# Optimization experiments

Hardware: AMD Instinct MI355X
Metric: run time of the kernel (lower is better)

Reference implementation:

```python
import jax, jax.numpy as jnp
import numpy as np
from jax import lax

B, LAT, NCLS, NGF, NC = 256, 100, 10, 128, 3
EPS = 1e-5


def _convt(x, w, stride, pad):
    # torch ConvTranspose2d(weight shape (Cin,Cout,k,k)) == lhs-dilated conv
    # with spatially flipped, in/out-swapped kernel and padding k-1-pad.
    k = w.shape[2]
    wt = jnp.flip(w, (2, 3)).transpose(1, 0, 2, 3)  # (Cout, Cin, k, k)
    p = k - 1 - pad
    return lax.conv_general_dilated(x, wt, (1, 1), [(p, p), (p, p)],
                                    lhs_dilation=(stride, stride),
                                    dimension_numbers=('NCHW', 'OIHW', 'NCHW'))


def _cconvt(xr, xi, wr, wi, br, bi, stride, pad):
    # complex transposed conv decomposed into 4 real convs (as torch does)
    yr = _convt(xr, wr, stride, pad) - _convt(xi, wi, stride, pad) + br[None, :, None, None]
    yi = _convt(xr, wi, stride, pad) + _convt(xi, wr, stride, pad) + bi[None, :, None, None]
    return yr, yi


def _cbn(xr, xi, grr, gri, gii, br, bi):
    # complex batchnorm: 2x2 covariance whitening over (N,H,W) + affine
    ax = (0, 2, 3)
    bc = lambda v: v[None, :, None, None]
    xr = xr - bc(xr.mean(ax))
    xi = xi - bc(xi.mean(ax))
    crr = (xr * xr).mean(ax) + EPS
    cii = (xi * xi).mean(ax) + EPS
    cri = (xr * xi).mean(ax)
    s = jnp.sqrt(crr * cii - cri * cri)          # sqrt(det)
    t = jnp.sqrt(crr + cii + 2.0 * s)            # sqrt(trace + 2 sqrt(det))
    inv = 1.0 / (s * t)
    rrr = (cii + s) * inv
    rii = (crr + s) * inv
    rri = -cri * inv
    yr = bc(rrr) * xr + bc(rri) * xi
    yi = bc(rri) * xr + bc(rii) * xi
    out_r = bc(grr) * yr + bc(gri) * yi + bc(br)
    out_i = bc(gri) * yr + bc(gii) * yi + bc(bi)
    return out_r, out_i


def _forward(noise_re, noise_im, labels, emb,
             w1r, w1i, b1r, b1i, g1rr, g1ri, g1ii, n1br, n1bi,
             w2r, w2i, b2r, b2i, g2rr, g2ri, g2ii, n2br, n2bi,
             w3r, w3i, b3r, b3i, g3rr, g3ri, g3ii, n3br, n3bi,
             w4r, w4i, b4r, b4i):
    lab = emb[labels][:, :, None, None]  # (B, NCLS, 1, 1); embedding is real
    xr = jnp.concatenate([noise_re, lab], axis=1)
    xi = jnp.concatenate([noise_im, jnp.zeros_like(lab)], axis=1)
    # 1x1 -> 4x4
    xr, xi = _cconvt(xr, xi, w1r, w1i, b1r, b1i, 1, 0)
    xr, xi = _cbn(xr, xi, g1rr, g1ri, g1ii, n1br, n1bi)
    xr, xi = jax.nn.relu(xr), jax.nn.relu(xi)  # CReLU
    # 4x4 -> 8x8
    xr, xi = _cconvt(xr, xi, w2r, w2i, b2r, b2i, 2, 1)
    xr, xi = _cbn(xr, xi, g2rr, g2ri, g2ii, n2br, n2bi)
    xr, xi = jax.nn.relu(xr), jax.nn.relu(xi)
    # 8x8 -> 16x16
    xr, xi = _cconvt(xr, xi, w3r, w3i, b3r, b3i, 2, 1)
    xr, xi = _cbn(xr, xi, g3rr, g3ri, g3ii, n3br, n3bi)
    xr, xi = jax.nn.relu(xr), jax.nn.relu(xi)
    # 16x16 -> 32x32
    xr, xi = _cconvt(xr, xi, w4r, w4i, b4r, b4i, 2, 1)
    return jnp.tanh(xr), jnp.tanh(xi)  # CTanh


def setup_inputs() -> dict:
    key = jax.random.key(0)
    ks = iter(jax.random.split(key, 40))
    rn = lambda shape, s: jax.random.normal(next(ks), shape, jnp.float32) * s
    d = {}
    d['noise_re'] = rn((B, LAT, 1, 1), 1.0)
    d['noise_im'] = rn((B, LAT, 1, 1), 1.0)
    d['labels'] = jax.random.randint(next(ks), (B,), 0, NCLS, jnp.int32)
    d['emb'] = rn((NCLS, NCLS), 1.0)
    chans = [(LAT + NCLS, NGF * 4), (NGF * 4, NGF * 2), (NGF * 2, NGF), (NGF, NC)]
    for i, (ci, co) in enumerate(chans, 1):
        d[f'w{i}r'] = rn((ci, co, 4, 4), 0.02)
        d[f'w{i}i'] = rn((ci, co, 4, 4), 0.02)
        d[f'b{i}r'] = jnp.zeros((co,), jnp.float32)
        d[f'b{i}i'] = jnp.zeros((co,), jnp.float32)
        if i < 4:
            d[f'g{i}rr'] = jnp.full((co,), 0.70710678, jnp.float32)
            d[f'g{i}ri'] = jnp.zeros((co,), jnp.float32)
            d[f'g{i}ii'] = jnp.full((co,), 0.70710678, jnp.float32)
            d[f'n{i}br'] = jnp.zeros((co,), jnp.float32)
            d[f'n{i}bi'] = jnp.zeros((co,), jnp.float32)
    return d


def reference(noise_re, noise_im, labels, emb,
              w1r, w1i, b1r, b1i, g1rr, g1ri, g1ii, n1br, n1bi,
              w2r, w2i, b2r, b2i, g2rr, g2ri, g2ii, n2br, n2bi,
              w3r, w3i, b3r, b3i, g3rr, g3ri, g3ii, n3br, n3bi,
              w4r, w4i, b4r, b4i):
    out_r, out_i = _forward(noise_re, noise_im, labels, emb,
                            w1r, w1i, b1r, b1i, g1rr, g1ri, g1ii, n1br, n1bi,
                            w2r, w2i, b2r, b2i, g2rr, g2ri, g2ii, n2br, n2bi,
                            w3r, w3i, b3r, b3i, g3rr, g3ri, g3ii, n3br, n3bi,
                            w4r, w4i, b4r, b4i)
    return out_r + 1j * out_i  # complex64 (B, NC, 32, 32)
```

## Files before the change

### kernel.cpp

```cpp
#include <hip/hip_runtime.h>
#include <hip/hip_bf16.h>
#include <math.h>

#define BATCH 256
#define LAT 100
#define NCLS 10
#define CIN0 110
#define C1 512
#define C2 256
#define C3 128
#define NCH 3
#define EPS 1e-5f

typedef __hip_bfloat16 bf16;
typedef short bf16x8 __attribute__((ext_vector_type(8)));
typedef float f32x4 __attribute__((ext_vector_type(4)));

__device__ __forceinline__ float b2f(bf16 v) { return __bfloat162float(v); }
__device__ __forceinline__ bf16 f2b(float v) { return __float2bfloat16(v); }
__device__ __forceinline__ float s2f(short s) {
    unsigned u = ((unsigned)(unsigned short)s) << 16;
    return __builtin_bit_cast(float, u);
}
__device__ __forceinline__ short f2s(float f) {
    bf16 b = __float2bfloat16(f);
    return *(short*)&b;
}

#define NB_W1 14336
#define NB_W2 32768
#define NB_W3 8192
#define NB_W4 256
#define NB_X0 224

__device__ __forceinline__ void w1prep_body(const float* wr, const float* wi, bf16* B, int idx) {
    if (idx >= 16384 * 224) return;
    int n = idx / 224, k = idx - n * 224;
    int p = n >> 10, cop = n & 1023;
    int pk = k >= 112; int ci = k - pk * 112;
    float v = 0.f;
    if (ci < CIN0) {
        int co = (cop < C1) ? cop : cop - C1;
        size_t widx = ((size_t)ci * C1 + co) * 16 + p;
        float vr = wr[widx], vi = wi[widx];
        v = (cop < C1) ? (pk ? -vi : vr) : (pk ? vr : vi);
    }
    B[idx] = f2b(v);
}

template<int CIN, int N>
__device__ __forceinline__ void wprep_panel_body(const float* wr, const float* wi, bf16* W,
                                                 size_t idx) {
    constexpr int K = 4 * CIN, TWOK = 8 * CIN;
    size_t per_cls = (size_t)2 * N * TWOK;
    if (idx >= 4 * per_cls) return;
    int cls = (int)(idx / per_cls);
    size_t r = idx - (size_t)cls * per_cls;
    size_t chunk_nb = (size_t)TWOK * 128;
    int nb = (int)(r / chunk_nb);
    int r2 = (int)(r - (size_t)nb * chunk_nb);
    int kb = r2 >> 12;
    int w = r2 & 4095;
    int f = w >> 9;
    int l = (w >> 3) & 63;
    int j = w & 7;
    int n = nb * 128 + (f >> 2) * 64 + (f & 3) * 16 + (l & 15);
    int k = kb * 32 + (l >> 4) * 8 + j;
    int py = cls >> 1, px = cls & 1;
    int p = k >= K; int kk = k - p * K;
    int t = kk / CIN, ci = kk - t * CIN;
    int a = t >> 1, e = t & 1;
    int kh = py ? (a ? 2 : 0) : (a ? 3 : 1);
    int kw = px ? (e ? 2 : 0) : (e ? 3 : 1);
    int co = (n < N) ? n : n - N;
    size_t widx = ((size_t)ci * N + co) * 16 + kh * 4 + kw;
    float vr = wr[widx], vi = wi[widx];
    float v = (n < N) ? (p ? -vi : vr) : (p ? vr : vi);
    W[idx] = f2b(v);
}

__device__ __forceinline__ void wprep4_body(const float* wr, const float* wi, bf16* W, int idx) {
    if (idx >= 65536) return;
    int cls = idx >> 14, rem = idx & 16383;
    int py = cls >> 1, px = cls & 1;
    int n = rem >> 10, k = rem & 1023;
    float v = 0.f;
    if (n < NCH) {
        int p = k >= 512; int kk = k - p * 512;
        int t = kk >> 7, ci = kk & 127;
        int a = t >> 1, e = t & 1;
        int kh = py ? (a ? 2 : 0) : (a ? 3 : 1);
        int kw = px ? (e ? 2 : 0) : (e ? 3 : 1);
        size_t widx = ((size_t)ci * NCH + n) * 16 + kh * 4 + kw;
        v = p ? -wi[widx] : wr[widx];
    }
    W[idx] = f2b(v);
}

__device__ __forceinline__ void x0_body(const float* nre, const float* nim,
                                        const int* labels, const float* emb,
                                        bf16* A, int idx) {
    if (idx >= BATCH * 224) return;
    int b = idx / 224, k = idx - b * 224;
    int p = k >= 112; int ci = k - p * 112;
    float v = 0.f;
    if (ci < CIN0) {
        if (!p) v = (ci < LAT) ? nre[b * LAT + ci] : emb[labels[b] * NCLS + (ci - LAT)];
        else    v = (ci < LAT) ? nim[b * LAT + ci] : 0.f;
    }
    A[idx] = f2b(v);
}

__global__ void prep_combined(const float* __restrict__ w1r, const float* __restrict__ w1i,
                              const float* __restrict__ w2r, const float* __restrict__ w2i,
                              const float* __restrict__ w3r, const float* __restrict__ w3i,
                              const float* __restrict__ w4r, const float* __restrict__ w4i,
                              const float* __restrict__ nre, const float* __restrict__ nim,
                              const int* __restrict__ labels, const float* __restrict__ emb,
                              bf16* __restrict__ B1, bf16* __restrict__ W2all,
                              bf16* __restrict__ W3all, bf16* __restrict__ W4all,
                              bf16* __restrict__ x0bf) {
    int bid = blockIdx.x;
    if (bid < NB_W1) {
        w1prep_body(w1r, w1i, B1, bid * 256 + threadIdx.x);
    } else if (bid < NB_W1 + NB_W2) {
        wprep_panel_body<C1, C2>(w2r, w2i, W2all, (size_t)(bid - NB_W1) * 256 + threadIdx.x);
    } else if (bid < NB_W1 + NB_W2 + NB_W3) {
        wprep_panel_body<C2, C3>(w3r, w3i, W3all, (size_t)(bid - NB_W1 - NB_W2) * 256 + threadIdx.x);
    } else if (bid < NB_W1 + NB_W2 + NB_W3 + NB_W4) {
        wprep4_body(w4r, w4i, W4all, (bid - NB_W1 - NB_W2 - NB_W3) * 256 + threadIdx.x);
    } else {
        x0_body(nre, nim, labels, emb, x0bf,
                (bid - NB_W1 - NB_W2 - NB_W3 - NB_W4) * 256 + threadIdx.x);
    }
}

__global__ __launch_bounds__(256, 1) void gemm1(
    const bf16* __restrict__ A, const bf16* __restrict__ B,
    const float* __restrict__ b1r, const float* __restrict__ b1i,
    bf16* __restrict__ Y) {
    __shared__ short As[128][40];
    __shared__ short Bs[128][40];
    const int tid = threadIdx.x;
    const int mBase = blockIdx.x * 128, nBase = blockIdx.y * 128;
    const int wid = tid >> 6, lane = tid & 63;
    const int wm = (wid >> 1) * 64, wn = (wid & 1) * 64;
    const int lm = lane & 15, lq = lane >> 4;

    f32x4 acc[4][4] = {};

    for (int k0 = 0; k0 < 224; k0 += 32) {
#pragma unroll
        for (int it = 0; it < 2; ++it) {
            int slot = tid + it * 256;
            int row = slot >> 2, kc = (slot & 3) * 8;
            int k = k0 + kc;
            *(uint4*)(&As[row][kc]) = *(const uint4*)(A + (size_t)(mBase + row) * 224 + k);
            *(uint4*)(&Bs[row][kc]) = *(const uint4*)(B + (size_t)(nBase + row) * 224 + k);
        }
        __syncthreads();
        bf16x8 af[4], bfr[4];
#pragma unroll
        for (int s = 0; s < 4; ++s) {
            af[s]  = *(const bf16x8*)(&As[wm + s * 16 + lm][lq * 8]);
            bfr[s] = *(const bf16x8*)(&Bs[wn + s * 16 + lm][lq * 8]);
        }
#pragma unroll
        for (int sm = 0; sm < 4; ++sm)
#pragma unroll
            for (int sn = 0; sn < 4; ++sn)
                acc[sm][sn] = __builtin_amdgcn_mfma_f32_16x16x32_bf16(af[sm], bfr[sn], acc[sm][sn], 0, 0, 0);
        __syncthreads();
    }

#pragma unroll
    for (int sm = 0; sm < 4; ++sm) {
#pragma unroll
        for (int v = 0; v < 4; ++v) {
            int m = mBase + wm + sm * 16 + lq * 4 + v;
#pragma unroll
            for (int sn = 0; sn < 4; ++sn) {
                int n = nBase + wn + sn * 16 + lm;
                int cop = n & 1023;
                float bias = (cop < C1) ? b1r[cop] : b1i[cop - C1];
                Y[(size_t)m * 16384 + n] = f2b(acc[sm][sn][v] + bias);
            }
        }
    }
}

__global__ void bn_stats_v(const bf16* __restrict__ Y, float* __restrict__ P,
                           int C, int logG, int rowsPerSlice) {
    const int tid = threadIdx.x;
    const int G = 1 << logG;
    const int g = tid & (G - 1);
    const int slice = tid >> logG;
    const int nsl = 256 >> logG;
    const int r0 = blockIdx.x * rowsPerSlice * nsl + slice * rowsPerSlice;
    const int CC = 2 * C;

    float sr[8] = {}, si[8] = {}, srr[8] = {}, sii[8] = {}, sri[8] = {};
    for (int r = r0; r < r0 + rowsPerSlice; ++r) {
        const bf16* p = Y + (size_t)r * CC + g * 8;
        bf16x8 vr8 = *(const bf16x8*)p;
        bf16x8 vi8 = *(const bf16x8*)(p + C);
#pragma unroll
        for (int j = 0; j < 8; ++j) {
            float vr = s2f(vr8[j]), vi = s2f(vi8[j]);
            sr[j] += vr; si[j] += vi;
            srr[j] += vr * vr; sii[j] += vi * vi; sri[j] += vr * vi;
        }
    }
    __shared__ float red[5][512];
    for (int i = tid; i < 5 * 512; i += 256) ((float*)red)[i] = 0.f;
    __syncthreads();
#pragma unroll
    for (int j = 0; j < 8; ++j) {
        int c = g * 8 + j;
        atomicAdd(&red[0][c], sr[j]);
        atomicAdd(&red[1][c], si[j]);
        atomicAdd(&red[2][c], srr[j]);
        atomicAdd(&red[3][c], sii[j]);
        atomicAdd(&red[4][c], sri[j]);
    }
    __syncthreads();
    for (int c = tid; c < C; c += 256) {
        float* dst = P + ((size_t)blockIdx.x * C + c) * 5;
        dst[0] = red[0][c]; dst[1] = red[1][c]; dst[2] = red[2][c];
        dst[3] = red[3][c]; dst[4] = red[4][c];
    }
}

__global__ void bn_coef_v(const float* __restrict__ P,
                          const float* __restrict__ grr, const float* __restrict__ gri,
                          const float* __restrict__ gii,
                          const float* __restrict__ betar, const float* __restrict__ betai,
                          float* __restrict__ coef, int C, float invN) {
    int c = blockIdx.x * blockDim.x + threadIdx.x;
    if (c >= C) return;
    float sr = 0, si = 0, srr = 0, sii = 0, sri = 0;
    for (int b = 0; b < 128; ++b) {
        const float* p = P + ((size_t)b * C + c) * 5;
        sr += p[0]; si += p[1]; srr += p[2]; sii += p[3]; sri += p[4];
    }
    float mr = sr * invN, mi = si * invN;
    float crr = srr * invN - mr * mr + EPS;
    float cii = sii * invN - mi * mi + EPS;
    float cri = sri * invN - mr * mi;
    float s = sqrtf(crr * cii - cri * cri);
    float t = sqrtf(crr + cii + 2.f * s);
    float inv = 1.f / (s * t);
    float rrr = (cii + s) * inv, rii = (crr + s) * inv, rri = -cri * inv;
    float Grr = grr[c], Gri = gri[c], Gii = gii[c];
    float arr = Grr * rrr + Gri * rri, ari = Grr * rri + Gri * rii;
    float air = Gri * rrr + Gii * rri, aii = Gri * rri + Gii * rii;
    coef[0 * C + c] = arr;
    coef[1 * C + c] = ari;
    coef[2 * C + c] = betar[c] - arr * mr - ari * mi;
    coef[3 * C + c] = air;
    coef[4 * C + c] = aii;
    coef[5 * C + c] = betai[c] - air * mr - aii * mi;
}

__global__ void bn_apply_v(bf16* __restrict__ Y, const float* __restrict__ coef,
                           int C, int logG, int total) {
    int idx = blockIdx.x * 256 + threadIdx.x;
    if (idx >= total) return;
    int G = 1 << logG;
    int g = idx & (G - 1);
    size_t base = (size_t)(idx >> logG) * 2 * C + g * 8;
    bf16x8 vr8 = *(const bf16x8*)(Y + base);
    bf16x8 vi8 = *(const bf16x8*)(Y + base + C);
    bf16x8 or8, oi8;
#pragma unroll
    for (int j = 0; j < 8; ++j) {
        int c = g * 8 + j;
        float vr = s2f(vr8[j]), vi = s2f(vi8[j]);
        float orr = fmaxf(coef[0 * C + c] * vr + coef[1 * C + c] * vi + coef[2 * C + c], 0.f);
        float oii = fmaxf(coef[3 * C + c] * vr + coef[4 * C + c] * vi + coef[5 * C + c], 0.f);
        or8[j] = f2s(orr); oi8[j] = f2s(oii);
    }
    *(bf16x8*)(Y + base) = or8;
    *(bf16x8*)(Y + base + C) = oi8;
}

template<int CIN, int S, int N>
__global__ __launch_bounds__(256, 2) void gemm_convt_bd(
    const bf16* __restrict__ X, const bf16* __restrict__ Wall,
    const float* __restrict__ biasr, const float* __restrict__ biasi,
    bf16* __restrict__ Y) {
    constexpr int K = 4 * CIN, TWOK = 8 * CIN, C2I = 2 * CIN, C2O = 2 * N, HOUT = 2 * S;
    constexpr int NSTEP = TWOK / 32;
    constexpr int CPS = CIN / 32;
    constexpr int LOG_CPS = (CIN == 512) ? 4 : 3;
    __shared__ short As[2][128][40];
    const int cls = blockIdx.z;
    const int py = cls >> 1, px = cls & 1;
    const int tid = threadIdx.x;
    const int mBase = blockIdx.x * 128, nBase = blockIdx.y * 128;
    const int wid = tid >> 6, lane = tid & 63;
    const int wm = (wid >> 1) * 64, wn = (wid & 1) * 64;
    const int lm = lane & 15, lq = lane >> 4;
    const int dh0 = py ? 1 : 0, dh1 = py ? 0 : -1;
    const int dw0 = px ? 1 : 0, dw1 = px ? 0 : -1;

    const bf16* Wp = Wall
        + ((size_t)(cls * (C2O / 128) + blockIdx.y) * (TWOK / 32)) * 4096
        + ((wn >> 6) * 4) * 512 + lane * 8;

    int rowA[2], kcA[2];
    long offT[2][4];
#pragma unroll
    for (int it = 0; it < 2; ++it) {
        int slot = tid + it * 256;
        rowA[it] = slot >> 2; kcA[it] = (slot & 3) * 8;
        int m = mBase + rowA[it];
        int b = m / (S * S); int rem = m - b * (S * S);
        int i = rem / S, j = rem % S;
#pragma unroll
        for (int t = 0; t < 4; ++t) {
            int a = t >> 1, e = t & 1;
            int ih = i + (a ? dh1 : dh0);
            int iw = j + (e ? dw1 : dw0);
            offT[it][t] = ((unsigned)ih < (unsigned)S && (unsigned)iw < (unsigned)S)
                ? (long)((b * S + ih) * S + iw) * C2I : -1L;
        }
    }

    auto loadA = [&](int kb, uint4* av) {
        int sec = kb >> LOG_CPS;
        int ci0 = (kb & (CPS - 1)) << 5;
        int p = sec >> 2, t = sec & 3;
#pragma unroll
        for (int it = 0; it < 2; ++it) {
            long o = offT[it][t];
            uint4 v = {0u, 0u, 0u, 0u};
            if (o >= 0)
                v = *(const uint4*)(X + o + p * CIN + ci0 + kcA[it]);
            av[it] = v;
        }
    };

    f32x4 acc[4][4] = {};
    bf16x8 bq[4];
#pragma unroll
    for (int sn = 0; sn < 4; ++sn) bq[sn] = *(const bf16x8*)(Wp + sn * 512);

    {
        uint4 av[2];
        loadA(0, av);
#pragma unroll
        for (int it = 0; it < 2; ++it) *(uint4*)(&As[0][rowA[it]][kcA[it]]) = av[it];
    }
    __syncthreads();

    for (int ks = 0; ks < NSTEP; ++ks) {
        const int cur = ks & 1;
        uint4 av[2];
        if (ks + 1 < NSTEP) loadA(ks + 1, av);
        bf16x8 bcur[4];
#pragma unroll
        for (int sn = 0; sn < 4; ++sn) bcur[sn] = bq[sn];
        if (ks + 1 < NSTEP) {
            const bf16* Wn = Wp + (size_t)(ks + 1) * 4096;
#pragma unroll
            for (int sn = 0; sn < 4; ++sn) bq[sn] = *(const bf16x8*)(Wn + sn * 512);
        }
        bf16x8 af[4];
#pragma unroll
        for (int s = 0; s < 4; ++s)
            af[s] = *(const bf16x8*)(&As[cur][wm + s * 16 + lm][lq * 8]);
#pragma unroll
        for (int sm = 0; sm < 4; ++sm)
#pragma unroll
            for (int sn = 0; sn < 4; ++sn)
                acc[sm][sn] = __builtin_amdgcn_mfma_f32_16x16x32_bf16(af[sm], bcur[sn], acc[sm][sn], 0, 0, 0);
        if (ks + 1 < NSTEP) {
#pragma unroll
            for (int it = 0; it < 2; ++it) *(uint4*)(&As[1 - cur][rowA[it]][kcA[it]]) = av[it];
        }
        __syncthreads();
    }

#pragma unroll
    for (int sm = 0; sm < 4; ++sm) {
#pragma unroll
        for (int v = 0; v < 4; ++v) {
            int m = mBase + wm + sm * 16 + lq * 4 + v;
            int b = m / (S * S); int rem = m - b * (S * S);
            int i = rem / S, j = rem % S;
            int oh = 2 * i + py, ow = 2 * j + px;
            size_t rowoff = (size_t)((b * HOUT + oh) * HOUT + ow) * C2O;
#pragma unroll
            for (int sn = 0; sn < 4; ++sn) {
                int n = nBase + wn + sn * 16 + lm;
                float bias = (n < N) ? biasr[n] : biasi[n - N];
                Y[rowoff + n] = f2b(acc[sm][sn][v] + bias);
            }
        }
    }
}

__global__ __launch_bounds__(256, 2) void conv4_mfma(
    const bf16* __restrict__ X, const bf16* __restrict__ Wall,
    const float* __restrict__ br, float* __restrict__ out) {
    constexpr int CIN = 128, S = 16, K = 512, TWOK = 1024, C2I = 256;
    constexpr int CPS = 4, LOG_CPS = 2;
    __shared__ short As[128][40];
    __shared__ short Bs[16][40];
    const int cls = blockIdx.z;
    const int py = cls >> 1, px = cls & 1;
    const bf16* W = Wall + (size_t)cls * 16 * TWOK;
    const int tid = threadIdx.x;
    const int mBase = blockIdx.x * 128;
    const int wid = tid >> 6, lane = tid & 63;
    const int wm = wid * 32;
    const int lm = lane & 15, lq = lane >> 4;
    const int dh0 = py ? 1 : 0, dh1 = py ? 0 : -1;
    const int dw0 = px ? 1 : 0, dw1 = px ? 0 : -1;

    int rowA[2], kcA[2];
    long offT[2][4];
#pragma unroll
    for (int it = 0; it < 2; ++it) {
        int slot = tid + it * 256;
        rowA[it] = slot >> 2; kcA[it] = (slot & 3) * 8;
        int m = mBase + rowA[it];
        int b = m >> 8; int rem = m & 255;
        int i = rem >> 4, j = rem & 15;
#pragma unroll
        for (int t = 0; t < 4; ++t) {
            int a = t >> 1, e = t & 1;
            int ih = i + (a ? dh1 : dh0);
            int iw = j + (e ? dw1 : dw0);
            offT[it][t] = ((unsigned)ih < (unsigned)S && (unsigned)iw < (unsigned)S)
                ? (long)((b * S + ih) * S + iw) * C2I : -1L;
        }
    }

    f32x4 acc[2] = {};

    for (int kb = 0; kb < TWOK / 32; ++kb) {
        int sec = kb >> LOG_CPS;
        int ci0 = (kb & (CPS - 1)) << 5;
        int p = sec >> 2, t = sec & 3;
#pragma unroll
        for (int it = 0; it < 2; ++it) {
            long o = offT[it][t];
            uint4 v = {0u, 0u, 0u, 0u};
            if (o >= 0)
                v = *(const uint4*)(X + o + p * CIN + ci0 + kcA[it]);
            *(uint4*)(&As[rowA[it]][kcA[it]]) = v;
        }
        if (tid < 64) {
            int row = tid >> 2, kc = (tid & 3) * 8;
            uint4 w = *(const uint4*)(W + (size_t)row * TWOK + kb * 32 + kc);
            *(uint4*)(&Bs[row][kc]) = w;
        }
        __syncthreads();
        bf16x8 bfr = *(const bf16x8*)(&Bs[lm][lq * 8]);
        bf16x8 af0 = *(const bf16x8*)(&As[wm + lm][lq * 8]);
        bf16x8 af1 = *(const bf16x8*)(&As[wm + 16 + lm][lq * 8]);
        acc[0] = __builtin_amdgcn_mfma_f32_16x16x32_bf16(af0, bfr, acc[0], 0, 0, 0);
        acc[1] = __builtin_amdgcn_mfma_f32_16x16x32_bf16(af1, bfr, acc[1], 0, 0, 0);
        __syncthreads();
    }

    int n = lm;
    if (n < NCH) {
        float bias = br[n];
#pragma unroll
        for (int s = 0; s < 2; ++s) {
#pragma unroll
            for (int v = 0; v < 4; ++v) {
                int m = mBase + wm + s * 16 + lq * 4 + v;
                int b = m >> 8; int rem = m & 255;
                int i = rem >> 4, j = rem & 15;
                int oh = 2 * i + py, ow = 2 * j + px;
                out[((size_t)(b * NCH + n) * 32 + oh) * 32 + ow] = tanhf(acc[s][v] + bias);
            }
        }
    }
}

extern "C" void kernel_launch(void* const* d_in, const int* in_sizes, int n_in,
                              void* d_out, int out_size, void* d_ws, size_t ws_size,
                              hipStream_t stream) {
    const float* noise_re = (const float*)d_in[0];
    const float* noise_im = (const float*)d_in[1];
    const int*   labels   = (const int*)d_in[2];
    const float* emb      = (const float*)d_in[3];
    const float* w1r = (const float*)d_in[4],  *w1i = (const float*)d_in[5];
    const float* b1r = (const float*)d_in[6],  *b1i = (const float*)d_in[7];
    const float* g1rr = (const float*)d_in[8], *g1ri = (const float*)d_in[9], *g1ii = (const float*)d_in[10];
    const float* n1br = (const float*)d_in[11], *n1bi = (const float*)d_in[12];
    const float* w2r = (const float*)d_in[13], *w2i = (const float*)d_in[14];
    const float* b2r = (const float*)d_in[15], *b2i = (const float*)d_in[16];
    const float* g2rr = (const float*)d_in[17], *g2ri = (const float*)d_in[18], *g2ii = (const float*)d_in[19];
    const float* n2br = (const float*)d_in[20], *n2bi = (const float*)d_in[21];
    const float* w3r = (const float*)d_in[22], *w3i = (const float*)d_in[23];
    const float* b3r = (const float*)d_in[24], *b3i = (const float*)d_in[25];
    const float* g3rr = (const float*)d_in[26], *g3ri = (const float*)d_in[27], *g3ii = (const float*)d_in[28];
    const float* n3br = (const float*)d_in[29], *n3bi = (const float*)d_in[30];
    const float* w4r = (const float*)d_in[31], *w4i = (const float*)d_in[32];
    const float* b4r = (const float*)d_in[33], *b4i = (const float*)d_in[34];

    char* ws = (char*)d_ws;
    bf16* y3cl = (bf16*)ws;
    bf16* x1cl = (bf16*)ws;
    bf16* B1    = (bf16*)(ws + 8388608);
    float* part12 = (float*)(ws + 8388608);
    bf16* W2all = (bf16*)(ws + 15728640);
    bf16* y2cl  = (bf16*)(ws + 33554432);
    bf16* W3all = (bf16*)(ws + 50331648);
    float* part3 = (float*)(ws + 50331648);
    float* coef1 = (float*)(ws + 54525952);
    float* coef2 = (float*)(ws + 54538240);
    float* coef3 = (float*)(ws + 54544384);
    bf16* x0bf  = (bf16*)(ws + 54547456);
    bf16* W4all = (bf16*)(ws + 54662144);

    prep_combined<<<NB_W1 + NB_W2 + NB_W3 + NB_W4 + NB_X0, 256, 0, stream>>>(
        w1r, w1i, w2r, w2i, w3r, w3i, w4r, w4i,
        noise_re, noise_im, labels, emb,
        B1, W2all, W3all, W4all, x0bf);

    gemm1<<<dim3(2, 128), 256, 0, stream>>>(x0bf, B1, b1r, b1i, x1cl);

    bn_stats_v<<<128, 256, 0, stream>>>(x1cl, part12, C1, 6, 8);
    bn_coef_v<<<2, 256, 0, stream>>>(part12, g1rr, g1ri, g1ii, n1br, n1bi, coef1, C1, 1.f / 4096.f);
    bn_apply_v<<<1024, 256, 0, stream>>>(x1cl, coef1, C1, 6, 4096 * 64);

    gemm_convt_bd<C1, 4, C2><<<dim3(32, 4, 4), 256, 0, stream>>>(x1cl, W2all, b2r, b2i, y2cl);

    bn_stats_v<<<128, 256, 0, stream>>>(y2cl, part12, C2, 5, 16);
    bn_coef_v<<<1, 256, 0, stream>>>(part12, g2rr, g2ri, g2ii, n2br, n2bi, coef2, C2, 1.f / 16384.f);
    bn_apply_v<<<2048, 256, 0, stream>>>(y2cl, coef2, C2, 5, 16384 * 32);

    gemm_convt_bd<C2, 8, C3><<<dim3(128, 2, 4), 256, 0, stream>>>(y2cl, W3all, b3r, b3i, y3cl);

    bn_stats_v<<<128, 256, 0, stream>>>(y3cl, part3, C3, 4, 32);
    bn_coef_v<<<1, 256, 0, stream>>>(part3, g3rr, g3ri, g3ii, n3br, n3bi, coef3, C3, 1.f / 65536.f);
    bn_apply_v<<<4096, 256, 0, stream>>>(y3cl, coef3, C3, 4, 65536 * 16);

    conv4_mfma<<<dim3(512, 1, 4), 256, 0, stream>>>(y3cl, W4all, b4r, (float*)d_out);
}
```

Measured before the change: 544.0 us.

## Fuse BN statistics into GEMM epilogues and coefficient math into apply

Weight columns are interleaved as real/imag pairs so each GEMM epilogue can accumulate per-channel complex BN sums (including the cross term via a lane shuffle) and atomically add them to global stats. This removes the separate bn_stats and bn_coef kernels and their extra read pass over each activation tensor. The apply kernel now recomputes the whitening coefficients per element from the raw sums. The final conv4 kernel also doubles its M tile per block. The cost is global float atomics, a per-launch memset, redundant per-element coefficient math, and more register pressure in the epilogue.

```diff
diff --git a/kernel.cpp b/kernel.cpp
--- a/kernel.cpp
+++ b/kernel.cpp
@@ -36,14 +36,15 @@
 __device__ __forceinline__ void w1prep_body(const float* wr, const float* wi, bf16* B, int idx) {
     if (idx >= 16384 * 224) return;
     int n = idx / 224, k = idx - n * 224;
-    int p = n >> 10, cop = n & 1023;
+    int p = n >> 10;
+    int c = (n & 1023) >> 1;
+    int part = n & 1;
     int pk = k >= 112; int ci = k - pk * 112;
     float v = 0.f;
     if (ci < CIN0) {
-        int co = (cop < C1) ? cop : cop - C1;
-        size_t widx = ((size_t)ci * C1 + co) * 16 + p;
+        size_t widx = ((size_t)ci * C1 + c) * 16 + p;
         float vr = wr[widx], vi = wi[widx];
-        v = (cop < C1) ? (pk ? -vi : vr) : (pk ? vr : vi);
+        v = (part == 0) ? (pk ? -vi : vr) : (pk ? vr : vi);
     }
     B[idx] = f2b(v);
 }
@@ -64,18 +65,18 @@
     int f = w >> 9;
     int l = (w >> 3) & 63;
     int j = w & 7;
-    int n = nb * 128 + (f >> 2) * 64 + (f & 3) * 16 + (l & 15);
+    int n_virt = nb * 128 + (f >> 2) * 64 + (f & 3) * 16 + (l & 15);
     int k = kb * 32 + (l >> 4) * 8 + j;
+    int c = n_virt >> 1, part = n_virt & 1;
     int py = cls >> 1, px = cls & 1;
     int p = k >= K; int kk = k - p * K;
     int t = kk / CIN, ci = kk - t * CIN;
     int a = t >> 1, e = t & 1;
     int kh = py ? (a ? 2 : 0) : (a ? 3 : 1);
     int kw = px ? (e ? 2 : 0) : (e ? 3 : 1);
-    int co = (n < N) ? n : n - N;
-    size_t widx = ((size_t)ci * N + co) * 16 + kh * 4 + kw;
+    size_t widx = ((size_t)ci * N + c) * 16 + kh * 4 + kw;
     float vr = wr[widx], vi = wi[widx];
-    float v = (n < N) ? (p ? -vi : vr) : (p ? vr : vi);
+    float v = (part == 0) ? (p ? -vi : vr) : (p ? vr : vi);
     W[idx] = f2b(v);
 }
 
@@ -135,10 +136,35 @@
     }
 }
 
+__device__ __forceinline__ void epi_stats_flush(float* red, float* Sstat, int Cn,
+                                                int cBaseGlobal, int tid,
+                                                const int* clArr, const float* s1,
+                                                const float* s2, const float* sp, int isRe) {
+    for (int i = tid; i < 320; i += 256) red[i] = 0.f;
+    __syncthreads();
+#pragma unroll
+    for (int sn = 0; sn < 4; ++sn) {
+        int cl = clArr[sn];
+        if (isRe) {
+            atomicAdd(&red[cl * 5 + 0], s1[sn]);
+            atomicAdd(&red[cl * 5 + 2], s2[sn]);
+            atomicAdd(&red[cl * 5 + 4], sp[sn]);
+        } else {
+            atomicAdd(&red[cl * 5 + 1], s1[sn]);
+            atomicAdd(&red[cl * 5 + 3], s2[sn]);
+        }
+    }
+    __syncthreads();
+    for (int i = tid; i < 320; i += 256) {
+        int cl = i / 5, st = i - cl * 5;
+        atomicAdd(&Sstat[st * Cn + cBaseGlobal + cl], red[i]);
+    }
+}
+
 __global__ __launch_bounds__(256, 1) void gemm1(
     const bf16* __restrict__ A, const bf16* __restrict__ B,
     const float* __restrict__ b1r, const float* __restrict__ b1i,
-    bf16* __restrict__ Y) {
+    bf16* __restrict__ Y, float* __restrict__ Sstat) {
     __shared__ short As[128][40];
     __shared__ short Bs[128][40];
     const int tid = threadIdx.x;
@@ -173,6 +199,13 @@
         __syncthreads();
     }
 
+    const int pos = nBase >> 10;
+    float s1[4] = {}, s2[4] = {}, sp[4] = {};
+    int clArr[4];
+#pragma unroll
+    for (int sn = 0; sn < 4; ++sn) clArr[sn] = (wn + sn * 16 + lm) >> 1;
+    const int part = lm & 1;
+
 #pragma unroll
     for (int sm = 0; sm < 4; ++sm) {
 #pragma unroll
@@ -181,89 +214,24 @@
 #pragma unroll
             for (int sn = 0; sn < 4; ++sn) {
                 int n = nBase + wn + sn * 16 + lm;
-                int cop = n & 1023;
-                float bias = (cop < C1) ? b1r[cop] : b1i[cop - C1];
-                Y[(size_t)m * 16384 + n] = f2b(acc[sm][sn][v] + bias);
+                int c = (n & 1023) >> 1;
+                float bias = part ? b1i[c] : b1r[c];
+                float val = acc[sm][sn][v] + bias;
+                float pv = __shfl_xor(val, 1, 64);
+                s1[sn] += val; s2[sn] += val * val;
+                if (!part) sp[sn] += val * pv;
+                Y[(size_t)m * 16384 + (pos << 10) + part * 512 + c] = f2b(val);
             }
         }
     }
-}
-
-__global__ void bn_stats_v(const bf16* __restrict__ Y, float* __restrict__ P,
-                           int C, int logG, int rowsPerSlice) {
-    const int tid = threadIdx.x;
-    const int G = 1 << logG;
-    const int g = tid & (G - 1);
-    const int slice = tid >> logG;
-    const int nsl = 256 >> logG;
-    const int r0 = blockIdx.x * rowsPerSlice * nsl + slice * rowsPerSlice;
-    const int CC = 2 * C;
-
-    float sr[8] = {}, si[8] = {}, srr[8] = {}, sii[8] = {}, sri[8] = {};
-    for (int r = r0; r < r0 + rowsPerSlice; ++r) {
-        const bf16* p = Y + (size_t)r * CC + g * 8;
-        bf16x8 vr8 = *(const bf16x8*)p;
-        bf16x8 vi8 = *(const bf16x8*)(p + C);
-#pragma unroll
-        for (int j = 0; j < 8; ++j) {
-            float vr = s2f(vr8[j]), vi = s2f(vi8[j]);
-            sr[j] += vr; si[j] += vi;
-            srr[j] += vr * vr; sii[j] += vi * vi; sri[j] += vr * vi;
-        }
-    }
-    __shared__ float red[5][512];
-    for (int i = tid; i < 5 * 512; i += 256) ((float*)red)[i] = 0.f;
-    __syncthreads();
-#pragma unroll
-    for (int j = 0; j < 8; ++j) {
-        int c = g * 8 + j;
-        atomicAdd(&red[0][c], sr[j]);
-        atomicAdd(&red[1][c], si[j]);
-        atomicAdd(&red[2][c], srr[j]);
-        atomicAdd(&red[3][c], sii[j]);
-        atomicAdd(&red[4][c], sri[j]);
-    }
-    __syncthreads();
-    for (int c = tid; c < C; c += 256) {
-        float* dst = P + ((size_t)blockIdx.x * C + c) * 5;
-        dst[0] = red[0][c]; dst[1] = red[1][c]; dst[2] = red[2][c];
-        dst[3] = red[3][c]; dst[4] = red[4][c];
-    }
-}
-
-__global__ void bn_coef_v(const float* __restrict__ P,
-                          const float* __restrict__ grr, const float* __restrict__ gri,
-                          const float* __restrict__ gii,
-                          const float* __restrict__ betar, const float* __restrict__ betai,
-                          float* __restrict__ coef, int C, float invN) {
-    int c = blockIdx.x * blockDim.x + threadIdx.x;
-    if (c >= C) return;
-    float sr = 0, si = 0, srr = 0, sii = 0, sri = 0;
-    for (int b = 0; b < 128; ++b) {
-        const float* p = P + ((size_t)b * C + c) * 5;
-        sr += p[0]; si += p[1]; srr += p[2]; sii += p[3]; sri += p[4];
-    }
-    float mr = sr * invN, mi = si * invN;
-    float crr = srr * invN - mr * mr + EPS;
-    float cii = sii * invN - mi * mi + EPS;
-    float cri = sri * invN - mr * mi;
-    float s = sqrtf(crr * cii - cri * cri);
-    float t = sqrtf(crr + cii + 2.f * s);
-    float inv = 1.f / (s * t);
-    float rrr = (cii + s) * inv, rii = (crr + s) * inv, rri = -cri * inv;
-    float Grr = grr[c], Gri = gri[c], Gii = gii[c];
-    float arr = Grr * rrr + Gri * rri, ari = Grr * rri + Gri * rii;
-    float air = Gri * rrr + Gii * rri, aii = Gri * rri + Gii * rii;
-    coef[0 * C + c] = arr;
-    coef[1 * C + c] = ari;
-    coef[2 * C + c] = betar[c] - arr * mr - ari * mi;
-    coef[3 * C + c] = air;
-    coef[4 * C + c] = aii;
-    coef[5 * C + c] = betai[c] - air * mr - aii * mi;
-}
-
-__global__ void bn_apply_v(bf16* __restrict__ Y, const float* __restrict__ coef,
-                           int C, int logG, int total) {
+    epi_stats_flush((float*)As, Sstat, C1, (nBase & 1023) >> 1, tid, clArr, s1, s2, sp, !part);
+}
+
+__global__ void bn_apply_v2(bf16* __restrict__ Y, const float* __restrict__ S,
+                            const float* __restrict__ grr, const float* __restrict__ gri,
+                            const float* __restrict__ gii,
+                            const float* __restrict__ betar, const float* __restrict__ betai,
+                            int C, int logG, int total, float invN) {
     int idx = blockIdx.x * 256 + threadIdx.x;
     if (idx >= total) return;
     int G = 1 << logG;
@@ -275,10 +243,23 @@
 #pragma unroll
     for (int j = 0; j < 8; ++j) {
         int c = g * 8 + j;
+        float sr = S[c], si = S[C + c], srr = S[2 * C + c], sii = S[3 * C + c], sri = S[4 * C + c];
+        float mr = sr * invN, mi = si * invN;
+        float crr = srr * invN - mr * mr + EPS;
+        float cii = sii * invN - mi * mi + EPS;
+        float cri = sri * invN - mr * mi;
+        float s = sqrtf(crr * cii - cri * cri);
+        float t = sqrtf(crr + cii + 2.f * s);
+        float inv = 1.f / (s * t);
+        float rrr = (cii + s) * inv, rii = (crr + s) * inv, rri = -cri * inv;
+        float Grr = grr[c], Gri = gri[c], Gii = gii[c];
+        float arr = Grr * rrr + Gri * rri, ari = Grr * rri + Gri * rii;
+        float air = Gri * rrr + Gii * rri, aii = Gri * rri + Gii * rii;
+        float cR = betar[c] - arr * mr - ari * mi;
+        float cI = betai[c] - air * mr - aii * mi;
         float vr = s2f(vr8[j]), vi = s2f(vi8[j]);
-        float orr = fmaxf(coef[0 * C + c] * vr + coef[1 * C + c] * vi + coef[2 * C + c], 0.f);
-        float oii = fmaxf(coef[3 * C + c] * vr + coef[4 * C + c] * vi + coef[5 * C + c], 0.f);
-        or8[j] = f2s(orr); oi8[j] = f2s(oii);
+        or8[j] = f2s(fmaxf(arr * vr + ari * vi + cR, 0.f));
+        oi8[j] = f2s(fmaxf(air * vr + aii * vi + cI, 0.f));
     }
     *(bf16x8*)(Y + base) = or8;
     *(bf16x8*)(Y + base + C) = oi8;
@@ -288,7 +269,7 @@
 __global__ __launch_bounds__(256, 2) void gemm_convt_bd(
     const bf16* __restrict__ X, const bf16* __restrict__ Wall,
     const float* __restrict__ biasr, const float* __restrict__ biasi,
-    bf16* __restrict__ Y) {
+    bf16* __restrict__ Y, float* __restrict__ Sstat) {
     constexpr int K = 4 * CIN, TWOK = 8 * CIN, C2I = 2 * CIN, C2O = 2 * N, HOUT = 2 * S;
     constexpr int NSTEP = TWOK / 32;
     constexpr int CPS = CIN / 32;
@@ -382,6 +363,12 @@
         __syncthreads();
     }
 
+    float s1[4] = {}, s2[4] = {}, sp[4] = {};
+    int clArr[4];
+#pragma unroll
+    for (int sn = 0; sn < 4; ++sn) clArr[sn] = (wn + sn * 16 + lm) >> 1;
+    const int part = lm & 1;
+
 #pragma unroll
     for (int sm = 0; sm < 4; ++sm) {
 #pragma unroll
@@ -394,35 +381,41 @@
 #pragma unroll
             for (int sn = 0; sn < 4; ++sn) {
                 int n = nBase + wn + sn * 16 + lm;
-                float bias = (n < N) ? biasr[n] : biasi[n - N];
-                Y[rowoff + n] = f2b(acc[sm][sn][v] + bias);
+                int c = n >> 1;
+                float bias = part ? biasi[c] : biasr[c];
+                float val = acc[sm][sn][v] + bias;
+                float pv = __shfl_xor(val, 1, 64);
+                s1[sn] += val; s2[sn] += val * val;
+                if (!part) sp[sn] += val * pv;
+                Y[rowoff + part * N + c] = f2b(val);
             }
         }
     }
+    epi_stats_flush((float*)As, Sstat, N, nBase >> 1, tid, clArr, s1, s2, sp, !part);
 }
 
 __global__ __launch_bounds__(256, 2) void conv4_mfma(
     const bf16* __restrict__ X, const bf16* __restrict__ Wall,
     const float* __restrict__ br, float* __restrict__ out) {
-    constexpr int CIN = 128, S = 16, K = 512, TWOK = 1024, C2I = 256;
+    constexpr int S = 16, TWOK = 1024, C2I = 256, CIN = 128;
     constexpr int CPS = 4, LOG_CPS = 2;
-    __shared__ short As[128][40];
+    __shared__ short As[256][40];
     __shared__ short Bs[16][40];
     const int cls = blockIdx.z;
     const int py = cls >> 1, px = cls & 1;
     const bf16* W = Wall + (size_t)cls * 16 * TWOK;
     const int tid = threadIdx.x;
-    const int mBase = blockIdx.x * 128;
+    const int mBase = blockIdx.x * 256;
     const int wid = tid >> 6, lane = tid & 63;
-    const int wm = wid * 32;
+    const int wm = wid * 64;
     const int lm = lane & 15, lq = lane >> 4;
     const int dh0 = py ? 1 : 0, dh1 = py ? 0 : -1;
     const int dw0 = px ? 1 : 0, dw1 = px ? 0 : -1;
 
-    int rowA[2], kcA[2];
-    long offT[2][4];
-#pragma unroll
-    for (int it = 0; it < 2; ++it) {
+    int rowA[4], kcA[4];
+    long offT[4][4];
+#pragma unroll
+    for (int it = 0; it < 4; ++it) {
         int slot = tid + it * 256;
         rowA[it] = slot >> 2; kcA[it] = (slot & 3) * 8;
         int m = mBase + rowA[it];
@@ -438,14 +431,14 @@
         }
     }
 
-    f32x4 acc[2] = {};
+    f32x4 acc[4] = {};
 
     for (int kb = 0; kb < TWOK / 32; ++kb) {
         int sec = kb >> LOG_CPS;
         int ci0 = (kb & (CPS - 1)) << 5;
         int p = sec >> 2, t = sec & 3;
 #pragma unroll
-        for (int it = 0; it < 2; ++it) {
+        for (int it = 0; it < 4; ++it) {
             long o = offT[it][t];
             uint4 v = {0u, 0u, 0u, 0u};
             if (o >= 0)
@@ -459,10 +452,11 @@
         }
         __syncthreads();
         bf16x8 bfr = *(const bf16x8*)(&Bs[lm][lq * 8]);
-        bf16x8 af0 = *(const bf16x8*)(&As[wm + lm][lq * 8]);
-        bf16x8 af1 = *(const bf16x8*)(&As[wm + 16 + lm][lq * 8]);
-        acc[0] = __builtin_amdgcn_mfma_f32_16x16x32_bf16(af0, bfr, acc[0], 0, 0, 0);
-        acc[1] = __builtin_amdgcn_mfma_f32_16x16x32_bf16(af1, bfr, acc[1], 0, 0, 0);
+#pragma unroll
+        for (int s = 0; s < 4; ++s) {
+            bf16x8 af = *(const bf16x8*)(&As[wm + s * 16 + lm][lq * 8]);
+            acc[s] = __builtin_amdgcn_mfma_f32_16x16x32_bf16(af, bfr, acc[s], 0, 0, 0);
+        }
         __syncthreads();
     }
 
@@ -470,7 +464,7 @@
     if (n < NCH) {
         float bias = br[n];
 #pragma unroll
-        for (int s = 0; s < 2; ++s) {
+        for (int s = 0; s < 4; ++s) {
 #pragma unroll
             for (int v = 0; v < 4; ++v) {
                 int m = mBase + wm + s * 16 + lq * 4 + v;
@@ -509,39 +503,33 @@
     bf16* y3cl = (bf16*)ws;
     bf16* x1cl = (bf16*)ws;
     bf16* B1    = (bf16*)(ws + 8388608);
-    float* part12 = (float*)(ws + 8388608);
     bf16* W2all = (bf16*)(ws + 15728640);
     bf16* y2cl  = (bf16*)(ws + 33554432);
     bf16* W3all = (bf16*)(ws + 50331648);
-    float* part3 = (float*)(ws + 50331648);
-    float* coef1 = (float*)(ws + 54525952);
-    float* coef2 = (float*)(ws + 54538240);
-    float* coef3 = (float*)(ws + 54544384);
     bf16* x0bf  = (bf16*)(ws + 54547456);
     bf16* W4all = (bf16*)(ws + 54662144);
+    float* S1 = (float*)(ws + 54793216);
+    float* S2 = (float*)(ws + 54803456);
+    float* S3 = (float*)(ws + 54808576);
+
+    (void)hipMemsetAsync(S1, 0, 17920, stream);
 
     prep_combined<<<NB_W1 + NB_W2 + NB_W3 + NB_W4 + NB_X0, 256, 0, stream>>>(
         w1r, w1i, w2r, w2i, w3r, w3i, w4r, w4i,
         noise_re, noise_im, labels, emb,
         B1, W2all, W3all, W4all, x0bf);
 
-    gemm1<<<dim3(2, 128), 256, 0, stream>>>(x0bf, B1, b1r, b1i, x1cl);
-
-    bn_stats_v<<<128, 256, 0, stream>>>(x1cl, part12, C1, 6, 8);
-    bn_coef_v<<<2, 256, 0, stream>>>(part12, g1rr, g1ri, g1ii, n1br, n1bi, coef1, C1, 1.f / 4096.f);
-    bn_apply_v<<<1024, 256, 0, stream>>>(x1cl, coef1, C1, 6, 4096 * 64);
-
-    gemm_convt_bd<C1, 4, C2><<<dim3(32, 4, 4), 256, 0, stream>>>(x1cl, W2all, b2r, b2i, y2cl);
-
-    bn_stats_v<<<128, 256, 0, stream>>>(y2cl, part12, C2, 5, 16);
-    bn_coef_v<<<1, 256, 0, stream>>>(part12, g2rr, g2ri, g2ii, n2br, n2bi, coef2, C2, 1.f / 16384.f);
-    bn_apply_v<<<2048, 256, 0, stream>>>(y2cl, coef2, C2, 5, 16384 * 32);
-
-    gemm_convt_bd<C2, 8, C3><<<dim3(128, 2, 4), 256, 0, stream>>>(y2cl, W3all, b3r, b3i, y3cl);
-
-    bn_stats_v<<<128, 256, 0, stream>>>(y3cl, part3, C3, 4, 32);
-    bn_coef_v<<<1, 256, 0, stream>>>(part3, g3rr, g3ri, g3ii, n3br, n3bi, coef3, C3, 1.f / 65536.f);
-    bn_apply_v<<<4096, 256, 0, stream>>>(y3cl, coef3, C3, 4, 65536 * 16);
-
-    conv4_mfma<<<dim3(512, 1, 4), 256, 0, stream>>>(y3cl, W4all, b4r, (float*)d_out);
-}
+    gemm1<<<dim3(2, 128), 256, 0, stream>>>(x0bf, B1, b1r, b1i, x1cl, S1);
+    bn_apply_v2<<<1024, 256, 0, stream>>>(x1cl, S1, g1rr, g1ri, g1ii, n1br, n1bi,
+                                          C1, 6, 4096 * 64, 1.f / 4096.f);
+
+    gemm_convt_bd<C1, 4, C2><<<dim3(32, 4, 4), 256, 0, stream>>>(x1cl, W2all, b2r, b2i, y2cl, S2);
+    bn_apply_v2<<<2048, 256, 0, stream>>>(y2cl, S2, g2rr, g2ri, g2ii, n2br, n2bi,
+                                          C2, 5, 16384 * 32, 1.f / 16384.f);
+
+    gemm_convt_bd<C2, 8, C3><<<dim3(128, 2, 4), 256, 0, stream>>>(y2cl, W3all, b3r, b3i, y3cl, S3);
+    bn_apply_v2<<<4096, 256, 0, stream>>>(y3cl, S3, g3rr, g3ri, g3ii, n3br, n3bi,
+                                          C3, 4, 65536 * 16, 1.f / 65536.f);
+
+    conv4_mfma<<<dim3(256, 1, 4), 256, 0, stream>>>(y3cl, W4all, b4r, (float*)d_out);
+}
```

Result: faster. 486.8 us (-10.5%).
